# Optimization experiments

Hardware: AMD Instinct MI355X
Metric: run time of the kernel (lower is better)

The kernel has to match this reference:

```python
import jax, jax.numpy as jnp
import numpy as np

N_NODES = 50000
N_EDGES = 800000
D_IN = 512
D_OUT = 512


def setup_inputs() -> dict:
    key = jax.random.key(0)
    k1, k2, k3, k4, k5 = jax.random.split(key, 5)
    x = jax.random.normal(k1, (N_NODES, D_IN), dtype=jnp.float32)
    # DGL GraphConv weight: [in_feats, out_feats], xavier-ish scale
    weight = jax.random.normal(k2, (D_IN, D_OUT), dtype=jnp.float32) * (1.0 / np.sqrt(D_IN))
    bias = jax.random.normal(k3, (D_OUT,), dtype=jnp.float32) * 0.01
    src = jax.random.randint(k4, (N_EDGES,), 0, N_NODES, dtype=jnp.int64)
    dst = jax.random.randint(k5, (N_EDGES,), 0, N_NODES, dtype=jnp.int64)
    return {"x": x, "weight": weight, "bias": bias, "src": src, "dst": dst}


def reference(x, weight, bias, src, dst):
    # DGL GraphConv with norm='none': sum messages from src -> dst, then linear.
    # (in_feats == out_feats so DGL aggregates first, then applies W; math is
    # identical either way.)
    msgs = x[src]                                            # [E, D_IN] gather
    agg = jax.ops.segment_sum(msgs, dst, num_segments=N_NODES)  # [N, D_IN]
    return agg @ weight + bias                               # [N, D_OUT]
```

## Files before the change

### kernel.cpp

```cpp
#include <hip/hip_runtime.h>
#include <hip/hip_bf16.h>

#define NN 50000
#define NE 800000
#define DD 512
#define NPAD 50048
#define STRIDE 96
#define LDA 36

typedef __attribute__((ext_vector_type(8))) short bf16x8;
typedef __attribute__((ext_vector_type(4))) float f32x4;
typedef __attribute__((ext_vector_type(8))) unsigned short u16x8;

__device__ __align__(16) unsigned short g_Wt[DD * DD];
__device__ __align__(16) unsigned short g_xb[(size_t)NN * DD];
__device__ __align__(16) unsigned short g_agg[(size_t)NPAD * DD];
__device__ unsigned g_cnt[NN];
__device__ int g_eidx[(size_t)NN * STRIDE];

static __device__ __forceinline__ unsigned short f2bf(float f) {
    unsigned u = __float_as_uint(f);
    u += 0x7fff + ((u >> 16) & 1);
    return (unsigned short)(u >> 16);
}
static __device__ __forceinline__ float bf2f(unsigned short u) {
    return __uint_as_float((unsigned)u << 16);
}

#define PB_CONV 12500
#define PB_WT   (PB_CONV + 1024)
#define PB_ZERO (PB_WT + 208)
__global__ void prep_all(const float* __restrict__ x, const float* __restrict__ W) {
    int b = blockIdx.x;
    int tid = threadIdx.x;
    if (b < PB_CONV) {
        size_t base = ((size_t)b * 256 + tid) * 8;
        float4 v0 = *(const float4*)(x + base);
        float4 v1 = *(const float4*)(x + base + 4);
        u16x8 o;
        o[0] = f2bf(v0.x); o[1] = f2bf(v0.y); o[2] = f2bf(v0.z); o[3] = f2bf(v0.w);
        o[4] = f2bf(v1.x); o[5] = f2bf(v1.y); o[6] = f2bf(v1.z); o[7] = f2bf(v1.w);
        *(u16x8*)(g_xb + base) = o;
    } else if (b < PB_WT) {
        int idx = (b - PB_CONV) * 256 + tid;
        int k = idx >> 9, n = idx & 511;
        g_Wt[n * DD + k] = f2bf(W[idx]);
    } else {
        int i = (b - PB_WT) * 256 + tid;
        if (i < NN) g_cnt[i] = 0;
        if (i < (NPAD - NN) * DD / 8) {
            u16x8 z = {0, 0, 0, 0, 0, 0, 0, 0};
            *(u16x8*)(g_agg + (size_t)NN * DD + (size_t)i * 8) = z;
        }
    }
}

__global__ void fill(const int* __restrict__ src, const int* __restrict__ dst) {
    int i = blockIdx.x * blockDim.x + threadIdx.x;
    if (i < NE) {
        int d = dst[i];
        unsigned pos = atomicAdd(&g_cnt[d], 1u);
        if (pos < STRIDE) g_eidx[(size_t)d * STRIDE + pos] = src[i];
    }
}

__global__ void aggregate() {
    int v = (blockIdx.x * blockDim.x + threadIdx.x) >> 6;
    int lane = threadIdx.x & 63;
    if (v >= NN) return;
    int deg = (int)g_cnt[v];
    if (deg > STRIDE) deg = STRIDE;
    const int* seg = g_eidx + (size_t)v * STRIDE;
    float a[8] = {0.f, 0.f, 0.f, 0.f, 0.f, 0.f, 0.f, 0.f};
    int i = 0;
    for (; i + 1 < deg; i += 2) {
        int s0 = seg[i], s1 = seg[i + 1];
        int4 q0 = *((const int4*)(g_xb + (size_t)s0 * DD) + lane);
        int4 q1 = *((const int4*)(g_xb + (size_t)s1 * DD) + lane);
        const unsigned short* u0 = (const unsigned short*)&q0;
        const unsigned short* u1 = (const unsigned short*)&q1;
#pragma unroll
        for (int j = 0; j < 8; ++j) a[j] += bf2f(u0[j]) + bf2f(u1[j]);
    }
    if (i < deg) {
        int s0 = seg[i];
        int4 q0 = *((const int4*)(g_xb + (size_t)s0 * DD) + lane);
        const unsigned short* u0 = (const unsigned short*)&q0;
#pragma unroll
        for (int j = 0; j < 8; ++j) a[j] += bf2f(u0[j]);
    }
    u16x8 o;
#pragma unroll
    for (int j = 0; j < 8; ++j) o[j] = f2bf(a[j]);
    *(u16x8*)(g_agg + (size_t)v * DD + lane * 8) = o;
}

__global__ __launch_bounds__(512) void gemm_kernel(float* __restrict__ out,
                                                   const float* __restrict__ bias) {
    __shared__ __align__(16) unsigned short As[128 * LDA];
    __shared__ __align__(16) unsigned short Bs[512 * LDA];
    const int m0 = blockIdx.x * 128;
    const int tid = threadIdx.x;
    const int wave = tid >> 6, lane = tid & 63;
    const int strip2 = wave >> 1;
    const int chalf = wave & 1;
    const int quad = lane >> 4, l16 = lane & 15;

    f32x4 acc[2][16];
#pragma unroll
    for (int s = 0; s < 2; ++s)
#pragma unroll
        for (int g = 0; g < 16; ++g) acc[s][g] = (f32x4){0.f, 0.f, 0.f, 0.f};

    for (int k0 = 0; k0 < DD; k0 += 32) {
        *(int4*)(&As[(tid >> 2) * LDA + (tid & 3) * 8]) =
            *(const int4*)(g_agg + (size_t)(m0 + (tid >> 2)) * DD + k0 + (tid & 3) * 8);
#pragma unroll
        for (int i = 0; i < 4; ++i) {
            int c = tid + i * 512;
            int n = c >> 2;
            int koff = (c & 3) << 3;
            *(int4*)(&Bs[n * LDA + koff]) = *(const int4*)(g_Wt + (size_t)n * DD + k0 + koff);
        }
        __syncthreads();
        bf16x8 a0 = *(const bf16x8*)(&As[(strip2 * 32 + l16) * LDA + quad * 8]);
        bf16x8 a1 = *(const bf16x8*)(&As[(strip2 * 32 + 16 + l16) * LDA + quad * 8]);
#pragma unroll
        for (int g = 0; g < 16; ++g) {
            bf16x8 b = *(const bf16x8*)(&Bs[(chalf * 256 + g * 16 + l16) * LDA + quad * 8]);
            acc[0][g] = __builtin_amdgcn_mfma_f32_16x16x32_bf16(a0, b, acc[0][g], 0, 0, 0);
            acc[1][g] = __builtin_amdgcn_mfma_f32_16x16x32_bf16(a1, b, acc[1][g], 0, 0, 0);
        }
        __syncthreads();
    }
#pragma unroll
    for (int s = 0; s < 2; ++s) {
        const int row_base = m0 + strip2 * 32 + s * 16 + quad * 4;
#pragma unroll
        for (int g = 0; g < 16; ++g) {
            int col = chalf * 256 + g * 16 + l16;
            float bv = bias[col];
#pragma unroll
            for (int r = 0; r < 4; ++r) {
                int row = row_base + r;
                if (row < NN) out[(size_t)row * DD + col] = acc[s][g][r] + bv;
            }
        }
    }
}

extern "C" void kernel_launch(void* const* d_in, const int* in_sizes, int n_in,
                              void* d_out, int out_size, void* d_ws, size_t ws_size,
                              hipStream_t stream) {
    const float* x    = (const float*)d_in[0];
    const float* W    = (const float*)d_in[1];
    const float* bias = (const float*)d_in[2];
    const int*   src  = (const int*)d_in[3];
    const int*   dst  = (const int*)d_in[4];
    float* out = (float*)d_out;
    (void)d_ws; (void)ws_size;

    prep_all<<<PB_ZERO, 256, 0, stream>>>(x, W);
    fill<<<(NE + 255) / 256, 256, 0, stream>>>(src, dst);
    aggregate<<<(NN * 64 + 255) / 256, 256, 0, stream>>>();
    gemm_kernel<<<NPAD / 128, 512, 0, stream>>>(out, bias);
}
```

Baseline: 432.5 us.

## Fuse edge bucketing into prep kernel, retile GEMM with direct-to-LDS loads

Edge bucketing moves into the prep kernel, and the counter zeroing becomes a memset, which removes one launch. The aggregation loop is unrolled to four gathers per iteration to raise memory-level parallelism, and several global accesses now use nontemporal loads and stores. The GEMM is retiled to 128x128 blocks of 256 threads with an XCD-aware block swizzle, and tiles are loaded with global_load_lds. The LDS layout is now unpadded, which risks bank conflicts, and each A row is now loaded by four blocks instead of one.

```diff
diff --git a/kernel.cpp b/kernel.cpp
--- a/kernel.cpp
+++ b/kernel.cpp
@@ -6,11 +6,11 @@
 #define DD 512
 #define NPAD 50048
 #define STRIDE 96
-#define LDA 36
 
 typedef __attribute__((ext_vector_type(8))) short bf16x8;
 typedef __attribute__((ext_vector_type(4))) float f32x4;
 typedef __attribute__((ext_vector_type(8))) unsigned short u16x8;
+typedef __attribute__((ext_vector_type(4))) int i32x4;
 
 __device__ __align__(16) unsigned short g_Wt[DD * DD];
 __device__ __align__(16) unsigned short g_xb[(size_t)NN * DD];
@@ -27,40 +27,37 @@
     return __uint_as_float((unsigned)u << 16);
 }
 
-#define PB_CONV 12500
-#define PB_WT   (PB_CONV + 1024)
-#define PB_ZERO (PB_WT + 208)
-__global__ void prep_all(const float* __restrict__ x, const float* __restrict__ W) {
+#define FB_FILL 3125
+#define FB_CONV (FB_FILL + 12500)
+#define FB_WT   (FB_CONV + 1024)
+#define FB_END  (FB_WT + 12)
+
+__global__ void prep_all(const float* __restrict__ x, const float* __restrict__ W,
+                         const int* __restrict__ src, const int* __restrict__ dst) {
     int b = blockIdx.x;
     int tid = threadIdx.x;
-    if (b < PB_CONV) {
-        size_t base = ((size_t)b * 256 + tid) * 8;
-        float4 v0 = *(const float4*)(x + base);
-        float4 v1 = *(const float4*)(x + base + 4);
+    if (b < FB_FILL) {
+        int i = b * 256 + tid;
+        int d = dst[i];
+        unsigned pos = atomicAdd(&g_cnt[d], 1u);
+        if (pos < STRIDE)
+            __builtin_nontemporal_store(src[i], &g_eidx[(size_t)d * STRIDE + pos]);
+    } else if (b < FB_CONV) {
+        size_t base = ((size_t)(b - FB_FILL) * 256 + tid) * 8;
+        f32x4 v0 = __builtin_nontemporal_load((const f32x4*)(x + base));
+        f32x4 v1 = __builtin_nontemporal_load((const f32x4*)(x + base) + 1);
         u16x8 o;
-        o[0] = f2bf(v0.x); o[1] = f2bf(v0.y); o[2] = f2bf(v0.z); o[3] = f2bf(v0.w);
-        o[4] = f2bf(v1.x); o[5] = f2bf(v1.y); o[6] = f2bf(v1.z); o[7] = f2bf(v1.w);
+        o[0] = f2bf(v0[0]); o[1] = f2bf(v0[1]); o[2] = f2bf(v0[2]); o[3] = f2bf(v0[3]);
+        o[4] = f2bf(v1[0]); o[5] = f2bf(v1[1]); o[6] = f2bf(v1[2]); o[7] = f2bf(v1[3]);
         *(u16x8*)(g_xb + base) = o;
-    } else if (b < PB_WT) {
-        int idx = (b - PB_CONV) * 256 + tid;
+    } else if (b < FB_WT) {
+        int idx = (b - FB_CONV) * 256 + tid;
         int k = idx >> 9, n = idx & 511;
         g_Wt[n * DD + k] = f2bf(W[idx]);
     } else {
-        int i = (b - PB_WT) * 256 + tid;
-        if (i < NN) g_cnt[i] = 0;
-        if (i < (NPAD - NN) * DD / 8) {
-            u16x8 z = {0, 0, 0, 0, 0, 0, 0, 0};
-            *(u16x8*)(g_agg + (size_t)NN * DD + (size_t)i * 8) = z;
-        }
-    }
-}
-
-__global__ void fill(const int* __restrict__ src, const int* __restrict__ dst) {
-    int i = blockIdx.x * blockDim.x + threadIdx.x;
-    if (i < NE) {
-        int d = dst[i];
-        unsigned pos = atomicAdd(&g_cnt[d], 1u);
-        if (pos < STRIDE) g_eidx[(size_t)d * STRIDE + pos] = src[i];
+        int i = (b - FB_WT) * 256 + tid;
+        u16x8 z = {0, 0, 0, 0, 0, 0, 0, 0};
+        *(u16x8*)(g_agg + (size_t)NN * DD + (size_t)i * 8) = z;
     }
 }
 
@@ -73,10 +70,24 @@
     const int* seg = g_eidx + (size_t)v * STRIDE;
     float a[8] = {0.f, 0.f, 0.f, 0.f, 0.f, 0.f, 0.f, 0.f};
     int i = 0;
+    for (; i + 3 < deg; i += 4) {
+        int s0 = seg[i], s1 = seg[i + 1], s2 = seg[i + 2], s3 = seg[i + 3];
+        i32x4 q0 = *((const i32x4*)(g_xb + ((size_t)s0 << 9)) + lane);
+        i32x4 q1 = *((const i32x4*)(g_xb + ((size_t)s1 << 9)) + lane);
+        i32x4 q2 = *((const i32x4*)(g_xb + ((size_t)s2 << 9)) + lane);
+        i32x4 q3 = *((const i32x4*)(g_xb + ((size_t)s3 << 9)) + lane);
+        const unsigned short* u0 = (const unsigned short*)&q0;
+        const unsigned short* u1 = (const unsigned short*)&q1;
+        const unsigned short* u2 = (const unsigned short*)&q2;
+        const unsigned short* u3 = (const unsigned short*)&q3;
+#pragma unroll
+        for (int j = 0; j < 8; ++j)
+            a[j] += (bf2f(u0[j]) + bf2f(u1[j])) + (bf2f(u2[j]) + bf2f(u3[j]));
+    }
     for (; i + 1 < deg; i += 2) {
         int s0 = seg[i], s1 = seg[i + 1];
-        int4 q0 = *((const int4*)(g_xb + (size_t)s0 * DD) + lane);
-        int4 q1 = *((const int4*)(g_xb + (size_t)s1 * DD) + lane);
+        i32x4 q0 = *((const i32x4*)(g_xb + ((size_t)s0 << 9)) + lane);
+        i32x4 q1 = *((const i32x4*)(g_xb + ((size_t)s1 << 9)) + lane);
         const unsigned short* u0 = (const unsigned short*)&q0;
         const unsigned short* u1 = (const unsigned short*)&q1;
 #pragma unroll
@@ -84,7 +95,7 @@
     }
     if (i < deg) {
         int s0 = seg[i];
-        int4 q0 = *((const int4*)(g_xb + (size_t)s0 * DD) + lane);
+        i32x4 q0 = *((const i32x4*)(g_xb + ((size_t)s0 << 9)) + lane);
         const unsigned short* u0 = (const unsigned short*)&q0;
 #pragma unroll
         for (int j = 0; j < 8; ++j) a[j] += bf2f(u0[j]);
@@ -92,58 +103,85 @@
     u16x8 o;
 #pragma unroll
     for (int j = 0; j < 8; ++j) o[j] = f2bf(a[j]);
-    *(u16x8*)(g_agg + (size_t)v * DD + lane * 8) = o;
-}
-
-__global__ __launch_bounds__(512) void gemm_kernel(float* __restrict__ out,
+    __builtin_nontemporal_store(*(i32x4*)&o, (i32x4*)(g_agg + ((size_t)v << 9)) + lane);
+}
+
+#define BM 128
+#define BN 128
+#define BK 32
+#define NWG ((NPAD / BM) * (DD / BN))
+
+__global__ __launch_bounds__(256) void gemm_kernel(float* __restrict__ out,
                                                    const float* __restrict__ bias) {
-    __shared__ __align__(16) unsigned short As[128 * LDA];
-    __shared__ __align__(16) unsigned short Bs[512 * LDA];
-    const int m0 = blockIdx.x * 128;
+    __shared__ __align__(16) unsigned short As[BM * BK];
+    __shared__ __align__(16) unsigned short Bs[BN * BK];
+
+    const int q = NWG >> 3, r = NWG & 7;
+    int xcd = blockIdx.x & 7, sub = blockIdx.x >> 3;
+    int swz = (xcd < r) ? xcd * (q + 1) + sub : r * (q + 1) + (xcd - r) * q + sub;
+    const int m0 = (swz >> 2) * BM;
+    const int n0 = (swz & 3) * BN;
+
     const int tid = threadIdx.x;
     const int wave = tid >> 6, lane = tid & 63;
-    const int strip2 = wave >> 1;
-    const int chalf = wave & 1;
+    const int wm = wave >> 1, wn = wave & 1;
     const int quad = lane >> 4, l16 = lane & 15;
 
-    f32x4 acc[2][16];
-#pragma unroll
-    for (int s = 0; s < 2; ++s)
-#pragma unroll
-        for (int g = 0; g < 16; ++g) acc[s][g] = (f32x4){0.f, 0.f, 0.f, 0.f};
-
-    for (int k0 = 0; k0 < DD; k0 += 32) {
-        *(int4*)(&As[(tid >> 2) * LDA + (tid & 3) * 8]) =
-            *(const int4*)(g_agg + (size_t)(m0 + (tid >> 2)) * DD + k0 + (tid & 3) * 8);
-#pragma unroll
-        for (int i = 0; i < 4; ++i) {
-            int c = tid + i * 512;
-            int n = c >> 2;
-            int koff = (c & 3) << 3;
-            *(int4*)(&Bs[n * LDA + koff]) = *(const int4*)(g_Wt + (size_t)n * DD + k0 + koff);
+    const int srow = lane >> 2;
+    const int skoff = (lane & 3) * 8;
+
+    f32x4 acc[4][4];
+#pragma unroll
+    for (int i = 0; i < 4; ++i)
+#pragma unroll
+        for (int j = 0; j < 4; ++j) acc[i][j] = (f32x4){0.f, 0.f, 0.f, 0.f};
+
+    const unsigned short* gA = g_agg + (size_t)m0 * DD;
+    const unsigned short* gB = g_Wt + (size_t)n0 * DD;
+
+    for (int k0 = 0; k0 < DD; k0 += BK) {
+#pragma unroll
+        for (int is = 0; is < 2; ++is) {
+            int row = wave * 32 + is * 16;
+            __builtin_amdgcn_global_load_lds(
+                (const __attribute__((address_space(1))) void*)
+                    (gA + (size_t)(row + srow) * DD + k0 + skoff),
+                (__attribute__((address_space(3))) void*)(As + row * BK), 16, 0, 0);
+            __builtin_amdgcn_global_load_lds(
+                (const __attribute__((address_space(1))) void*)
+                    (gB + (size_t)(row + srow) * DD + k0 + skoff),
+                (__attribute__((address_space(3))) void*)(Bs + row * BK), 16, 0, 0);
         }
         __syncthreads();
-        bf16x8 a0 = *(const bf16x8*)(&As[(strip2 * 32 + l16) * LDA + quad * 8]);
-        bf16x8 a1 = *(const bf16x8*)(&As[(strip2 * 32 + 16 + l16) * LDA + quad * 8]);
-#pragma unroll
-        for (int g = 0; g < 16; ++g) {
-            bf16x8 b = *(const bf16x8*)(&Bs[(chalf * 256 + g * 16 + l16) * LDA + quad * 8]);
-            acc[0][g] = __builtin_amdgcn_mfma_f32_16x16x32_bf16(a0, b, acc[0][g], 0, 0, 0);
-            acc[1][g] = __builtin_amdgcn_mfma_f32_16x16x32_bf16(a1, b, acc[1][g], 0, 0, 0);
+
+        bf16x8 af[4], bf[4];
+#pragma unroll
+        for (int t = 0; t < 4; ++t) {
+            af[t] = *(const bf16x8*)(&As[(wm * 64 + t * 16 + l16) * BK + quad * 8]);
+            bf[t] = *(const bf16x8*)(&Bs[(wn * 64 + t * 16 + l16) * BK + quad * 8]);
         }
+#pragma unroll
+        for (int am = 0; am < 4; ++am)
+#pragma unroll
+            for (int bn = 0; bn < 4; ++bn)
+                acc[am][bn] = __builtin_amdgcn_mfma_f32_16x16x32_bf16(
+                    af[am], bf[bn], acc[am][bn], 0, 0, 0);
         __syncthreads();
     }
-#pragma unroll
-    for (int s = 0; s < 2; ++s) {
-        const int row_base = m0 + strip2 * 32 + s * 16 + quad * 4;
-#pragma unroll
-        for (int g = 0; g < 16; ++g) {
-            int col = chalf * 256 + g * 16 + l16;
+
+#pragma unroll
+    for (int am = 0; am < 4; ++am) {
+        int row_base = m0 + wm * 64 + am * 16 + quad * 4;
+#pragma unroll
+        for (int bn = 0; bn < 4; ++bn) {
+            int col = n0 + wn * 64 + bn * 16 + l16;
             float bv = bias[col];
 #pragma unroll
-            for (int r = 0; r < 4; ++r) {
-                int row = row_base + r;
-                if (row < NN) out[(size_t)row * DD + col] = acc[s][g][r] + bv;
+            for (int rr = 0; rr < 4; ++rr) {
+                int rowi = row_base + rr;
+                if (rowi < NN)
+                    __builtin_nontemporal_store(acc[am][bn][rr] + bv,
+                                                out + (size_t)rowi * DD + col);
             }
         }
     }
@@ -160,8 +198,11 @@
     float* out = (float*)d_out;
     (void)d_ws; (void)ws_size;
 
-    prep_all<<<PB_ZERO, 256, 0, stream>>>(x, W);
-    fill<<<(NE + 255) / 256, 256, 0, stream>>>(src, dst);
+    static void* cnt_ptr = nullptr;
+    if (!cnt_ptr) (void)hipGetSymbolAddress(&cnt_ptr, HIP_SYMBOL(g_cnt));
+    hipMemsetAsync(cnt_ptr, 0, NN * sizeof(unsigned), stream);
+
+    prep_all<<<FB_END, 256, 0, stream>>>(x, W, src, dst);
     aggregate<<<(NN * 64 + 255) / 256, 256, 0, stream>>>();
-    gemm_kernel<<<NPAD / 128, 512, 0, stream>>>(out, bias);
-}
+    gemm_kernel<<<NWG, 256, 0, stream>>>(out, bias);
+}
```

New measurement: 459.3 us. +6.2%, slower.
